# Kernel tuning notes

Hardware: AMD Instinct MI355X
Metric: run time of the kernel (lower is better)

The kernel has to match this reference:

```python
import jax, jax.numpy as jnp
import numpy as np

NUM_CHANNEL = 2                      # channels per telescope group
K = 7                                # hexagonal kernel size
N_LEV = [2048, 512, 128, 32, 8]      # pixels per level (stride-2 hex pooling ~ /4)
CHS = [2, 64, 128, 256, 512]         # channel progression n1->n_features->n2->n3->n4


def _iconv(x, idx, w, b):
    # x: [B,C,Nin], idx: [K,Nout], w: [O,C,K] -> [B,O,Nout]
    g = x[:, :, idx]                              # gather neighbours [B,C,K,Nout]
    return jnp.einsum('bckn,ock->bon', g, w) + b[None, :, None]


def _ipool(x, idx):
    # IndexedMaxPool2d: gather then max over kernel positions
    return x[:, :, idx].max(axis=2)               # [B,C,Nout]


def _bn(x, gamma, beta, eps=1e-5):
    # train-mode BatchNorm1d over (batch, pixel) dims, biased variance (torch semantics)
    m = x.mean(axis=(0, 2), keepdims=True)
    v = x.var(axis=(0, 2), keepdims=True)
    return (x - m) / jnp.sqrt(v + eps) * gamma[None, :, None] + beta[None, :, None]


def setup_inputs() -> dict:
    key = jax.random.key(0)
    ks = jax.random.split(key, 40)
    ki = iter(range(40))
    nk = lambda: ks[next(ki)]
    B = 256
    inp = {"x": jax.random.normal(nk(), (B, 2 * NUM_CHANNEL, N_LEV[0]), jnp.float32)}
    for i in range(4):
        inp[f"idx_conv{i+1}"] = jax.random.randint(nk(), (K, N_LEV[i]), 0, N_LEV[i])
        inp[f"idx_pool{i+1}"] = jax.random.randint(nk(), (K, N_LEV[i + 1]), 0, N_LEV[i])
        fan = float(CHS[i] * K)
        inp[f"w{i+1}"] = jax.random.normal(nk(), (CHS[i + 1], CHS[i], K), jnp.float32) / np.float32(np.sqrt(fan))
        inp[f"b{i+1}"] = jnp.zeros((CHS[i + 1],), jnp.float32)
        inp[f"gamma{i+1}"] = jnp.ones((CHS[i + 1],), jnp.float32)
        inp[f"beta{i+1}"] = jnp.zeros((CHS[i + 1],), jnp.float32)
    F = N_LEV[4] * CHS[4]            # 8 * 512 = 4096
    H = F // 2                       # 2048
    inp["lin1_w"] = jax.random.normal(nk(), (H, F), jnp.float32) / np.float32(np.sqrt(F))
    inp["lin1_b"] = jnp.zeros((H,), jnp.float32)
    inp["gamma5"] = jnp.ones((H,), jnp.float32)
    inp["beta5"] = jnp.zeros((H,), jnp.float32)
    inp["lin2_w"] = jax.random.normal(nk(), (3, H), jnp.float32) / np.float32(np.sqrt(H))
    inp["lin2_b"] = jnp.zeros((3,), jnp.float32)
    return inp


def reference(x, idx_conv1, idx_pool1, idx_conv2, idx_pool2, idx_conv3, idx_pool3,
              idx_conv4, idx_pool4, w1, b1, gamma1, beta1, w2, b2, gamma2, beta2,
              w3, b3, gamma3, beta3, w4, b4, gamma4, beta4,
              lin1_w, lin1_b, gamma5, beta5, lin2_w, lin2_b):
    layers = [(idx_conv1, idx_pool1, w1, b1, gamma1, beta1),
              (idx_conv2, idx_pool2, w2, b2, gamma2, beta2),
              (idx_conv3, idx_pool3, w3, b3, gamma3, beta3),
              (idx_conv4, idx_pool4, w4, b4, gamma4, beta4)]
    T = x.shape[1] // NUM_CHANNEL    # number of telescope groups (static)
    outs = []
    for i in range(T):
        o = x[:, i * NUM_CHANNEL:(i + 1) * NUM_CHANNEL, :]
        for (ic, ip, w, b, g, be) in layers:
            # conv -> pool -> bn -> relu (dropout with p=0 is identity)
            o = jax.nn.relu(_bn(_ipool(_iconv(o, ic, w, b), ip), g, be))
        outs.append(o)
    o = jnp.stack(outs, 1).mean(axis=1)          # [B, 512, 8]
    o = o.reshape(o.shape[0], -1)                # [B, 4096]
    o = o @ lin1_w.T + lin1_b                    # [B, 2048]
    m = o.mean(axis=0)
    v = o.var(axis=0)
    o = (o - m) / jnp.sqrt(v + 1e-5) * gamma5 + beta5
    o = jax.nn.relu(o)
    o = o @ lin2_w.T + lin2_b                    # [B, 3]
    cls = jax.nn.log_softmax(o[:, :2], axis=1)   # targets: class=2 (log-softmax), energy=1 (raw)
    return jnp.concatenate([cls, o[:, 2:3]], axis=1)
```

## Files before the change

### kernel.cpp

```cpp
#include <hip/hip_runtime.h>
#include <math.h>

#define B 256
#define KW 7

typedef __bf16 bf16x8 __attribute__((ext_vector_type(8)));
typedef __bf16 bf16x4 __attribute__((ext_vector_type(4)));
typedef float  f32x4  __attribute__((ext_vector_type(4)));

__device__ __forceinline__ void block_reduce2(float& s, float& s2, float* lds) {
    for (int off = 32; off > 0; off >>= 1) {
        s  += __shfl_down(s,  off, 64);
        s2 += __shfl_down(s2, off, 64);
    }
    int wave = threadIdx.x >> 6;
    int lane = threadIdx.x & 63;
    if (lane == 0) { lds[wave * 2] = s; lds[wave * 2 + 1] = s2; }
    __syncthreads();
    if (threadIdx.x == 0) {
        s  = lds[0] + lds[2] + lds[4] + lds[6];
        s2 = lds[1] + lds[3] + lds[5] + lds[7];
    }
}

__global__ __launch_bounds__(256) void k_transpose(const float* __restrict__ x,
                                                   float* __restrict__ A0) {
    int bid = blockIdx.x;
    int nt  = bid & 63;
    int rem = bid >> 6;
    int ci  = rem & 1;
    int t   = rem >> 1;
    int n0  = nt * 32;
    __shared__ float lds[32][257];
    int tid = threadIdx.x;
    int nl  = tid & 31;
    int bq  = tid >> 5;
    int ch  = t * 2 + ci;
    for (int p = 0; p < 32; p++) {
        int b = bq + p * 8;
        lds[nl][b] = x[((size_t)b * 4 + ch) * 2048 + n0 + nl];
    }
    __syncthreads();
    for (int nl2 = 0; nl2 < 32; nl2++) {
        A0[(((size_t)t * 2048 + n0 + nl2) * 2 + ci) * B + tid] = lds[nl2][tid];
    }
}

__global__ __launch_bounds__(256) void k_convpool1(
    const float* __restrict__ act,
    float* __restrict__ P1,
    const float* __restrict__ w,
    const float* __restrict__ bias,
    const int* __restrict__ idx_conv,
    const int* __restrict__ idx_pool,
    float* __restrict__ part1c)
{
    const int Kt = 14, C_out = 64, N_in = 2048, N_out = 512;
    int bid   = blockIdx.x;
    int cot   = bid & 1;
    int colid = bid >> 1;
    int t     = colid / N_out;
    int np    = colid - t * N_out;
    int co0   = cot << 5;

    __shared__ float lds_g[14 * 256];
    __shared__ float lds_w[14 * 33];
    __shared__ int   lds_idx[KW];

    int tid = threadIdx.x;
    int cog = tid >> 6;
    int bl  = tid & 63;

    float pmax[8][4];
    #pragma unroll
    for (int i = 0; i < 8; i++)
        #pragma unroll
        for (int j = 0; j < 4; j++) pmax[i][j] = -INFINITY;

    const float* actT = act + (size_t)t * N_in * 2 * B;

    for (int kp = 0; kp < KW; kp++) {
        int nc = idx_pool[kp * N_out + np];
        if (tid < KW) lds_idx[tid] = idx_conv[tid * N_in + nc];

        float acc[8][4];
        #pragma unroll
        for (int i = 0; i < 8; i++)
            #pragma unroll
            for (int j = 0; j < 4; j++) acc[i][j] = 0.f;

        __syncthreads();
        for (int e = tid; e < 32 * Kt; e += 256) {
            int kk = e % Kt;
            int co = e / Kt;
            lds_w[kk * 33 + co] = w[(size_t)(co0 + co) * Kt + kk];
        }
        for (int r = 0; r < Kt; r++) {
            int ci  = r / KW;
            int k   = r - ci * KW;
            int col = lds_idx[k];
            lds_g[r * 256 + tid] = actT[((size_t)col * 2 + ci) * B + tid];
        }
        __syncthreads();
        for (int kk = 0; kk < Kt; kk++) {
            float g0 = lds_g[kk * 256 + bl];
            float g1 = lds_g[kk * 256 + bl + 64];
            float g2 = lds_g[kk * 256 + bl + 128];
            float g3 = lds_g[kk * 256 + bl + 192];
            const float* wr = lds_w + kk * 33 + cog * 8;
            #pragma unroll
            for (int i = 0; i < 8; i++) {
                float wv = wr[i];
                acc[i][0] = fmaf(wv, g0, acc[i][0]);
                acc[i][1] = fmaf(wv, g1, acc[i][1]);
                acc[i][2] = fmaf(wv, g2, acc[i][2]);
                acc[i][3] = fmaf(wv, g3, acc[i][3]);
            }
        }
        #pragma unroll
        for (int i = 0; i < 8; i++)
            #pragma unroll
            for (int j = 0; j < 4; j++) pmax[i][j] = fmaxf(pmax[i][j], acc[i][j]);
    }

    float* outp = P1 + (((size_t)t * N_out + np) * C_out + co0) * B;
    float* pblk = part1c + (size_t)bid * 64;
    #pragma unroll
    for (int i = 0; i < 8; i++) {
        int co = cog * 8 + i;
        float bv = bias[co0 + co];
        float s = 0.f, s2 = 0.f;
        #pragma unroll
        for (int j = 0; j < 4; j++) {
            float val = pmax[i][j] + bv;
            outp[(size_t)co * B + bl + 64 * j] = val;
            s  += val;
            s2 += val * val;
        }
        for (int o = 32; o > 0; o >>= 1) {
            s  += __shfl_down(s,  o, 64);
            s2 += __shfl_down(s2, o, 64);
        }
        if ((tid & 63) == 0) {
            pblk[co]      = s;
            pblk[32 + co] = s2;
        }
    }
}

__global__ __launch_bounds__(256) void k_finstats1(
    const float* __restrict__ part1c,
    const float* __restrict__ gamma, const float* __restrict__ beta,
    float* __restrict__ scale, float* __restrict__ shift)
{
    int idx = blockIdx.x;
    int t = idx >> 6, c = idx & 63;
    int cot = c >> 5, cl = c & 31;
    float s = 0.f, s2 = 0.f;
    for (int np = threadIdx.x; np < 512; np += 256) {
        const float* pp = part1c + (size_t)((t * 512 + np) * 2 + cot) * 64;
        s  += pp[cl];
        s2 += pp[32 + cl];
    }
    __shared__ float lds[8];
    block_reduce2(s, s2, lds);
    if (threadIdx.x == 0) {
        float cnt  = 512.f * 256.f;
        float m    = s / cnt;
        float var  = s2 / cnt - m * m;
        float istd = rsqrtf(var + 1e-5f);
        float g    = gamma[c];
        scale[idx] = istd * g;
        shift[idx] = beta[c] - m * istd * g;
    }
}

__global__ __launch_bounds__(256) void k_bnrelu1t(
    const float* __restrict__ P1,
    const float* __restrict__ sc, const float* __restrict__ sh,
    __bf16* __restrict__ act1)
{
    int bid = blockIdx.x;
    int t = bid >> 9;
    int b = threadIdx.x;
    const float* src = P1 + (size_t)bid * 64 * B;
    __bf16* dst = act1 + (size_t)bid * B * 64 + (size_t)b * 64;
    const float* scp = sc + t * 64;
    const float* shp = sh + t * 64;
    __bf16 vals[64];
    #pragma unroll
    for (int co = 0; co < 64; co++) {
        float v = src[co * B + b];
        vals[co] = (__bf16)fmaxf(fmaf(v, scp[co], shp[co]), 0.f);
    }
    #pragma unroll
    for (int j = 0; j < 8; j++)
        *(bf16x8*)(dst + j * 8) = *(bf16x8*)&vals[j * 8];
}

__global__ void k_wr(const float* __restrict__ w, __bf16* __restrict__ wr,
                     int C_in, int total) {
    int idx = blockIdx.x * 256 + threadIdx.x;
    if (idx >= total) return;
    int ci = idx % C_in;
    int r  = idx / C_in;
    int kt = r % 7;
    int co = r / 7;
    wr[idx] = (__bf16)w[((size_t)co * C_in + ci) * 7 + kt];
}

__global__ void k_cvt8(const float* __restrict__ src, __bf16* __restrict__ dst, int total8) {
    int idx = blockIdx.x * 256 + threadIdx.x;
    if (idx >= total8) return;
    const f32x4* s4 = (const f32x4*)(src + (size_t)idx * 8);
    f32x4 a = s4[0], b = s4[1];
    bf16x8 v;
    v[0] = (__bf16)a[0]; v[1] = (__bf16)a[1]; v[2] = (__bf16)a[2]; v[3] = (__bf16)a[3];
    v[4] = (__bf16)b[0]; v[5] = (__bf16)b[1]; v[6] = (__bf16)b[2]; v[7] = (__bf16)b[3];
    *(bf16x8*)(dst + (size_t)idx * 8) = v;
}

__global__ __launch_bounds__(256) void k_conv_mfma(
    const __bf16* __restrict__ act,
    float* __restrict__ convo,
    const __bf16* __restrict__ wr,
    const int* __restrict__ idx_conv,
    int C_in, int C_out, int N, int ci_shift, int t0)
{
    int nco = C_out >> 6;
    int bid = blockIdx.x;
    int cot = bid % nco;
    int rem = bid / nco;
    int n    = rem % N;
    int tloc = rem / N;
    int t    = t0 + tloc;
    int co0  = cot * 64;
    int Kt   = C_in * KW;

    int tid  = threadIdx.x;
    int wv   = tid >> 6;
    int lane = tid & 63;
    int quad = lane >> 4;
    int lid  = lane & 15;

    f32x4 acc[4][4];
    #pragma unroll
    for (int i = 0; i < 4; i++)
        #pragma unroll
        for (int j = 0; j < 4; j++) {
            acc[i][j][0] = 0.f; acc[i][j][1] = 0.f;
            acc[i][j][2] = 0.f; acc[i][j][3] = 0.f;
        }

    const __bf16* actT = act + (size_t)t * N * B * C_in;
    const __bf16* wbase = wr + (size_t)(co0 + lid) * Kt + quad * 8;

    for (int k0 = 0; k0 < Kt; k0 += 32) {
        int kt  = k0 >> ci_shift;
        int ci0 = k0 & (C_in - 1);
        int col = idx_conv[kt * N + n];

        bf16x8 afrag[4];
        #pragma unroll
        for (int rt = 0; rt < 4; rt++)
            afrag[rt] = *(const bf16x8*)(wbase + (size_t)rt * 16 * Kt + k0);

        bf16x8 bfrag[4];
        const __bf16* gbase = actT + ((size_t)col * B + wv * 64 + lid) * C_in + ci0 + quad * 8;
        #pragma unroll
        for (int bt = 0; bt < 4; bt++)
            bfrag[bt] = *(const bf16x8*)(gbase + (size_t)bt * 16 * C_in);

        #pragma unroll
        for (int rt = 0; rt < 4; rt++)
            #pragma unroll
            for (int bt = 0; bt < 4; bt++)
                acc[rt][bt] = __builtin_amdgcn_mfma_f32_16x16x32_bf16(
                    afrag[rt], bfrag[bt], acc[rt][bt], 0, 0, 0);
    }

    float* outp = convo + ((size_t)(tloc * N + n) * B) * C_out;
    #pragma unroll
    for (int rt = 0; rt < 4; rt++)
        #pragma unroll
        for (int bt = 0; bt < 4; bt++) {
            int b  = wv * 64 + bt * 16 + lid;
            int co = co0 + rt * 16 + quad * 4;
            *(f32x4*)(outp + (size_t)b * C_out + co) = acc[rt][bt];
        }
}

__global__ __launch_bounds__(256) void k_poolstats(
    const float* __restrict__ convo,
    float* __restrict__ P,
    const float* __restrict__ bias,
    const int* __restrict__ idx_pool,
    float* __restrict__ part,
    int C, int N, int No, int t0)
{
    int bid  = blockIdx.x;
    int bg   = bid & 3;
    int rem  = bid >> 2;
    int np   = rem % No;
    int tloc = rem / No;
    int t    = t0 + tloc;
    int cols[7];
    #pragma unroll
    for (int k = 0; k < 7; k++) cols[k] = idx_pool[k * No + np];
    const float* base = convo + (size_t)tloc * N * B * C;
    float* pout = P + ((size_t)(t * No + np) * B) * C;
    int tid = threadIdx.x;
    float s[2] = {0.f, 0.f}, s2[2] = {0.f, 0.f};
    int NC, c0, bstart, bstep, nb;
    if (C >= 256) { NC = C >> 8; c0 = tid;           bstart = 0;        bstep = 1; nb = 64; }
    else          { NC = 1;      c0 = tid & (C - 1); bstart = tid >> 7; bstep = 2; nb = 32; }
    for (int j = 0; j < NC; j++) {
        int c = c0 + j * 256;
        float bv = bias[c];
        for (int i = 0; i < nb; i++) {
            int b = bg * 64 + bstart + i * bstep;
            float m = -1e30f;
            #pragma unroll
            for (int k = 0; k < 7; k++) {
                float v = base[((size_t)cols[k] * B + b) * C + c];
                m = fmaxf(m, v);
            }
            float val = m + bv;
            pout[(size_t)b * C + c] = val;
            s[j] += val; s2[j] += val * val;
        }
    }
    float* pp = part + (size_t)((t * No + np) * 4 + bg) * 1024;
    for (int j = 0; j < NC; j++) {
        pp[tid + j * 256]       = s[j];
        pp[512 + tid + j * 256] = s2[j];
    }
}

__global__ __launch_bounds__(256) void k_finstats(
    const float* __restrict__ part,
    const float* __restrict__ gamma, const float* __restrict__ beta,
    float* __restrict__ scale, float* __restrict__ shift,
    int C, int No)
{
    int idx = blockIdx.x;
    int t = idx / C, c = idx - t * C;
    int SMAX   = C < 256 ? 256 : C;
    int nslice = SMAX / C;
    int nblk   = No * 4;
    int total  = nblk * nslice;
    const float* pbase = part + (size_t)(t * No * 4) * 1024;
    float s = 0.f, s2 = 0.f;
    for (int e = threadIdx.x; e < total; e += 256) {
        int blk = e / nslice;
        int j   = e - blk * nslice;
        const float* pp = pbase + (size_t)blk * 1024;
        int sl = c + j * C;
        s  += pp[sl];
        s2 += pp[512 + sl];
    }
    __shared__ float lds[8];
    block_reduce2(s, s2, lds);
    if (threadIdx.x == 0) {
        float cnt  = (float)No * 256.f;
        float m    = s / cnt;
        float var  = s2 / cnt - m * m;
        float istd = rsqrtf(var + 1e-5f);
        float g    = gamma[c];
        scale[idx] = istd * g;
        shift[idx] = beta[c] - m * istd * g;
    }
}

__global__ void k_bnrelu(const float* __restrict__ P, __bf16* __restrict__ act,
                         const float* __restrict__ scale, const float* __restrict__ shift,
                         int C, int total)
{
    int idx = blockIdx.x * 256 + threadIdx.x;
    if (idx >= total) return;
    int c = idx & (C - 1);
    int t = idx >= (total >> 1) ? 1 : 0;
    int tc = t * C + c;
    float v = P[idx];
    act[idx] = (__bf16)fmaxf(fmaf(v, scale[tc], shift[tc]), 0.f);
}

__global__ __launch_bounds__(256) void k_zbuild(const float* __restrict__ P4,
                                                const float* __restrict__ sc4,
                                                const float* __restrict__ sh4,
                                                __bf16* __restrict__ z)
{
    int b = blockIdx.x;
    int tid = threadIdx.x;
    for (int j = 0; j < 2; j++) {
        int c = tid + j * 256;
        float s0 = sc4[c],       h0 = sh4[c];
        float s1 = sc4[512 + c], h1 = sh4[512 + c];
        #pragma unroll
        for (int np = 0; np < 8; np++) {
            float v0 = P4[(((size_t)0 * 8 + np) * B + b) * 512 + c];
            float v1 = P4[(((size_t)1 * 8 + np) * B + b) * 512 + c];
            float y0 = fmaxf(fmaf(v0, s0, h0), 0.f);
            float y1 = fmaxf(fmaf(v1, s1, h1), 0.f);
            z[(size_t)b * 4096 + c * 8 + np] = (__bf16)(0.5f * (y0 + y1));
        }
    }
}

__global__ __launch_bounds__(256) void k_lin1_part(
    const __bf16* __restrict__ zb,
    const __bf16* __restrict__ w1b,
    float* __restrict__ partL)
{
    int ht = blockIdx.x >> 3;
    int ks = blockIdx.x & 7;
    int h0 = ht * 64;
    int f_beg = ks * 512, f_end = f_beg + 512;

    int tid  = threadIdx.x;
    int wv   = tid >> 6;
    int lane = tid & 63;
    int quad = lane >> 4;
    int lid  = lane & 15;

    f32x4 acc[4][4];
    #pragma unroll
    for (int i = 0; i < 4; i++)
        #pragma unroll
        for (int j = 0; j < 4; j++) {
            acc[i][j][0] = 0.f; acc[i][j][1] = 0.f;
            acc[i][j][2] = 0.f; acc[i][j][3] = 0.f;
        }

    const __bf16* wbase = w1b + (size_t)(h0 + lid) * 4096 + quad * 8;
    const __bf16* zbase = zb + ((size_t)(wv * 64 + lid)) * 4096 + quad * 8;

    for (int f0 = f_beg; f0 < f_end; f0 += 32) {
        bf16x8 afrag[4];
        #pragma unroll
        for (int rt = 0; rt < 4; rt++)
            afrag[rt] = *(const bf16x8*)(wbase + (size_t)rt * 16 * 4096 + f0);
        bf16x8 bfrag[4];
        #pragma unroll
        for (int bt = 0; bt < 4; bt++)
            bfrag[bt] = *(const bf16x8*)(zbase + (size_t)bt * 16 * 4096 + f0);
        #pragma unroll
        for (int rt = 0; rt < 4; rt++)
            #pragma unroll
            for (int bt = 0; bt < 4; bt++)
                acc[rt][bt] = __builtin_amdgcn_mfma_f32_16x16x32_bf16(
                    afrag[rt], bfrag[bt], acc[rt][bt], 0, 0, 0);
    }
    float* outp = partL + (size_t)ks * 2048 * B;
    #pragma unroll
    for (int rt = 0; rt < 4; rt++)
        #pragma unroll
        for (int bt = 0; bt < 4; bt++) {
            int b = wv * 64 + bt * 16 + lid;
            int h = h0 + rt * 16 + quad * 4;
            #pragma unroll
            for (int r = 0; r < 4; r++)
                outp[(size_t)(h + r) * B + b] = acc[rt][bt][r];
        }
}

__global__ __launch_bounds__(256) void k_redstats5(
    const float* __restrict__ partL,
    const float* __restrict__ b1,
    const float* __restrict__ gamma5, const float* __restrict__ beta5,
    float* __restrict__ o1,
    float* __restrict__ scale5, float* __restrict__ shift5)
{
    int h = blockIdx.x;
    int b = threadIdx.x;
    float v = b1[h];
    #pragma unroll
    for (int s = 0; s < 8; s++)
        v += partL[((size_t)s * 2048 + h) * B + b];
    o1[(size_t)h * B + b] = v;
    float s1 = v, s2 = v * v;
    __shared__ float lds[8];
    block_reduce2(s1, s2, lds);
    if (threadIdx.x == 0) {
        float m    = s1 * (1.f / 256.f);
        float var  = s2 * (1.f / 256.f) - m * m;
        float istd = rsqrtf(var + 1e-5f);
        float g    = gamma5[h];
        scale5[h]  = istd * g;
        shift5[h]  = beta5[h] - m * istd * g;
    }
}

__global__ __launch_bounds__(256) void k_final(
    const float* __restrict__ o1,
    const float* __restrict__ scale5, const float* __restrict__ shift5,
    const float* __restrict__ w2, const float* __restrict__ b2,
    float* __restrict__ out)
{
    int b = blockIdx.x;
    int tid = threadIdx.x;
    float s0 = 0.f, s1 = 0.f, s2v = 0.f;
    for (int h = tid; h < 2048; h += 256) {
        float y = fmaxf(fmaf(o1[(size_t)h * B + b], scale5[h], shift5[h]), 0.f);
        s0  = fmaf(y, w2[h],        s0);
        s1  = fmaf(y, w2[2048 + h], s1);
        s2v = fmaf(y, w2[4096 + h], s2v);
    }
    for (int off = 32; off > 0; off >>= 1) {
        s0  += __shfl_down(s0,  off, 64);
        s1  += __shfl_down(s1,  off, 64);
        s2v += __shfl_down(s2v, off, 64);
    }
    __shared__ float lds[12];
    int wave = tid >> 6, lane = tid & 63;
    if (lane == 0) { lds[wave * 3] = s0; lds[wave * 3 + 1] = s1; lds[wave * 3 + 2] = s2v; }
    __syncthreads();
    if (tid == 0) {
        float o0 = lds[0] + lds[3] + lds[6] + lds[9]  + b2[0];
        float oa = lds[1] + lds[4] + lds[7] + lds[10] + b2[1];
        float ob = lds[2] + lds[5] + lds[8] + lds[11] + b2[2];
        float m   = fmaxf(o0, oa);
        float lse = m + logf(expf(o0 - m) + expf(oa - m));
        out[b * 3 + 0] = o0 - lse;
        out[b * 3 + 1] = oa - lse;
        out[b * 3 + 2] = ob;
    }
}

extern "C" void kernel_launch(void* const* d_in, const int* in_sizes, int n_in,
                              void* d_out, int out_size, void* d_ws, size_t ws_size,
                              hipStream_t stream) {
    (void)in_sizes; (void)n_in; (void)out_size; (void)ws_size;

    const float* x   = (const float*)d_in[0];
    const int*   ic1 = (const int*)d_in[1];
    const int*   ip1 = (const int*)d_in[2];
    const float* pW1 = (const float*)d_in[3];
    const float* pB1 = (const float*)d_in[4];
    const float* pG1 = (const float*)d_in[5];
    const float* pE1 = (const float*)d_in[6];
    const int*   ic2 = (const int*)d_in[7];
    const int*   ip2 = (const int*)d_in[8];
    const float* pW2 = (const float*)d_in[9];
    const float* pB2 = (const float*)d_in[10];
    const float* pG2 = (const float*)d_in[11];
    const float* pE2 = (const float*)d_in[12];
    const int*   ic3 = (const int*)d_in[13];
    const int*   ip3 = (const int*)d_in[14];
    const float* pW3 = (const float*)d_in[15];
    const float* pB3 = (const float*)d_in[16];
    const float* pG3 = (const float*)d_in[17];
    const float* pE3 = (const float*)d_in[18];
    const int*   ic4 = (const int*)d_in[19];
    const int*   ip4 = (const int*)d_in[20];
    const float* pW4 = (const float*)d_in[21];
    const float* pB4 = (const float*)d_in[22];
    const float* pG4 = (const float*)d_in[23];
    const float* pE4 = (const float*)d_in[24];
    const float* lw1 = (const float*)d_in[25];
    const float* lb1 = (const float*)d_in[26];
    const float* g5  = (const float*)d_in[27];
    const float* e5  = (const float*)d_in[28];
    const float* lw2 = (const float*)d_in[29];
    const float* lb2 = (const float*)d_in[30];

    char* ws = (char*)d_ws;
    size_t off = 0;
    auto alloc = [&](size_t bytes) -> char* {
        char* p = ws + off;
        off += (bytes + 511) & ~(size_t)511;
        return p;
    };

    float*  A0    = (float*) alloc((size_t)2 * 2048 * 2 * B * 4);
    __bf16* act1  = (__bf16*)alloc((size_t)2 * 512 * B * 64 * 2);
    char*   U     =          alloc((size_t)512 * B * 128 * 4);
    float*  P1f   = (float*)U;
    float*  convX = (float*)U;
    float*  partL = (float*)U;
    float*  Pf    = (float*) alloc((size_t)2 * 128 * B * 128 * 4);
    __bf16* actS  = (__bf16*)alloc((size_t)2 * 128 * B * 128 * 2);
    __bf16* Wr2   = (__bf16*)alloc((size_t)128 * 448 * 2);
    __bf16* Wr3   = (__bf16*)alloc((size_t)256 * 896 * 2);
    __bf16* Wr4   = (__bf16*)alloc((size_t)512 * 1792 * 2);
    __bf16* w1b   = (__bf16*)alloc((size_t)2048 * 4096 * 2);
    __bf16* z     = (__bf16*)alloc((size_t)256 * 4096 * 2);
    float*  o1    = (float*) alloc((size_t)2048 * B * 4);
    float*  part  = (float*) alloc((size_t)2 * 128 * 4 * 1024 * 4);
    float*  part1c= (float*) alloc((size_t)2048 * 64 * 4);
    float*  sc1 = (float*)alloc(2 * 64 * 4);
    float*  sh1 = (float*)alloc(2 * 64 * 4);
    float*  sc2 = (float*)alloc(2 * 128 * 4);
    float*  sh2 = (float*)alloc(2 * 128 * 4);
    float*  sc3 = (float*)alloc(2 * 256 * 4);
    float*  sh3 = (float*)alloc(2 * 256 * 4);
    float*  sc4 = (float*)alloc(2 * 512 * 4);
    float*  sh4 = (float*)alloc(2 * 512 * 4);
    float*  sc5 = (float*)alloc(2048 * 4);
    float*  sh5 = (float*)alloc(2048 * 4);

    k_wr<<<(128 * 448 + 255) / 256, 256, 0, stream>>>(pW2, Wr2, 64, 128 * 448);
    k_wr<<<(256 * 896 + 255) / 256, 256, 0, stream>>>(pW3, Wr3, 128, 256 * 896);
    k_wr<<<(512 * 1792 + 255) / 256, 256, 0, stream>>>(pW4, Wr4, 256, 512 * 1792);
    k_cvt8<<<(2048 * 4096 / 8) / 256, 256, 0, stream>>>(lw1, w1b, 2048 * 4096 / 8);

    k_transpose<<<256, 256, 0, stream>>>(x, A0);

    k_convpool1<<<2048, 256, 0, stream>>>(A0, P1f, pW1, pB1, ic1, ip1, part1c);
    k_finstats1<<<2 * 64, 256, 0, stream>>>(part1c, pG1, pE1, sc1, sh1);
    k_bnrelu1t<<<2 * 512, 256, 0, stream>>>(P1f, sc1, sh1, act1);

    for (int t = 0; t < 2; t++) {
        k_conv_mfma<<<2 * 512, 256, 0, stream>>>(act1, convX, Wr2, ic2, 64, 128, 512, 6, t);
        k_poolstats<<<128 * 4, 256, 0, stream>>>(convX, Pf, pB2, ip2, part, 128, 512, 128, t);
    }
    k_finstats<<<2 * 128, 256, 0, stream>>>(part, pG2, pE2, sc2, sh2, 128, 128);
    k_bnrelu<<<(2 * 128 * B * 128) / 256, 256, 0, stream>>>(Pf, actS, sc2, sh2, 128, 2 * 128 * B * 128);

    k_conv_mfma<<<4 * 128 * 2, 256, 0, stream>>>(actS, convX, Wr3, ic3, 128, 256, 128, 7, 0);
    k_poolstats<<<2 * 32 * 4, 256, 0, stream>>>(convX, Pf, pB3, ip3, part, 256, 128, 32, 0);
    k_finstats<<<2 * 256, 256, 0, stream>>>(part, pG3, pE3, sc3, sh3, 256, 32);
    k_bnrelu<<<(2 * 32 * B * 256) / 256, 256, 0, stream>>>(Pf, actS, sc3, sh3, 256, 2 * 32 * B * 256);

    k_conv_mfma<<<8 * 32 * 2, 256, 0, stream>>>(actS, convX, Wr4, ic4, 256, 512, 32, 8, 0);
    k_poolstats<<<2 * 8 * 4, 256, 0, stream>>>(convX, Pf, pB4, ip4, part, 512, 32, 8, 0);
    k_finstats<<<2 * 512, 256, 0, stream>>>(part, pG4, pE4, sc4, sh4, 512, 8);

    k_zbuild<<<256, 256, 0, stream>>>(Pf, sc4, sh4, z);
    k_lin1_part<<<256, 256, 0, stream>>>(z, w1b, partL);
    k_redstats5<<<2048, 256, 0, stream>>>(partL, lb1, g5, e5, o1, sc5, sh5);
    k_final<<<256, 256, 0, stream>>>(o1, sc5, sh5, lw2, lb2, (float*)d_out);
}
```

Before: 763.4 us.

## Store conv outputs in bf16, widen conv tile to 128 channels, merge group launches

The MFMA conv kernel now computes 128 output channels per block instead of 64. This halves the number of times each gathered activation fragment is reloaded, at the cost of more accumulator registers. The conv output buffer switches from fp32 to bf16, halving its write and pool-read traffic, and the pooling kernel converts values back to float when it reads them. Because the bf16 buffer is smaller, both telescope groups now fit in the shared workspace, so layer 2 runs as one conv and one pool launch instead of a per-group loop. The risk is lower occupancy from 128 accumulator VGPRs and a bf16 rounding error before max-pool and batch norm.

```diff
diff --git a/kernel.cpp b/kernel.cpp
--- a/kernel.cpp
+++ b/kernel.cpp
@@ -222,20 +222,19 @@
 
 __global__ __launch_bounds__(256) void k_conv_mfma(
     const __bf16* __restrict__ act,
-    float* __restrict__ convo,
+    __bf16* __restrict__ convo,
     const __bf16* __restrict__ wr,
     const int* __restrict__ idx_conv,
-    int C_in, int C_out, int N, int ci_shift, int t0)
-{
-    int nco = C_out >> 6;
+    int C_in, int C_out, int N, int ci_shift)
+{
+    int nco = C_out >> 7;
     int bid = blockIdx.x;
     int cot = bid % nco;
     int rem = bid / nco;
-    int n    = rem % N;
-    int tloc = rem / N;
-    int t    = t0 + tloc;
-    int co0  = cot * 64;
-    int Kt   = C_in * KW;
+    int n   = rem % N;
+    int t   = rem / N;
+    int co0 = cot * 128;
+    int Kt  = C_in * KW;
 
     int tid  = threadIdx.x;
     int wv   = tid >> 6;
@@ -243,9 +242,9 @@
     int quad = lane >> 4;
     int lid  = lane & 15;
 
-    f32x4 acc[4][4];
-    #pragma unroll
-    for (int i = 0; i < 4; i++)
+    f32x4 acc[8][4];
+    #pragma unroll
+    for (int i = 0; i < 8; i++)
         #pragma unroll
         for (int j = 0; j < 4; j++) {
             acc[i][j][0] = 0.f; acc[i][j][1] = 0.f;
@@ -260,11 +259,6 @@
         int ci0 = k0 & (C_in - 1);
         int col = idx_conv[kt * N + n];
 
-        bf16x8 afrag[4];
-        #pragma unroll
-        for (int rt = 0; rt < 4; rt++)
-            afrag[rt] = *(const bf16x8*)(wbase + (size_t)rt * 16 * Kt + k0);
-
         bf16x8 bfrag[4];
         const __bf16* gbase = actT + ((size_t)col * B + wv * 64 + lid) * C_in + ci0 + quad * 8;
         #pragma unroll
@@ -272,42 +266,48 @@
             bfrag[bt] = *(const bf16x8*)(gbase + (size_t)bt * 16 * C_in);
 
         #pragma unroll
-        for (int rt = 0; rt < 4; rt++)
+        for (int rt = 0; rt < 8; rt++) {
+            bf16x8 afrag = *(const bf16x8*)(wbase + (size_t)rt * 16 * Kt + k0);
             #pragma unroll
             for (int bt = 0; bt < 4; bt++)
                 acc[rt][bt] = __builtin_amdgcn_mfma_f32_16x16x32_bf16(
-                    afrag[rt], bfrag[bt], acc[rt][bt], 0, 0, 0);
-    }
-
-    float* outp = convo + ((size_t)(tloc * N + n) * B) * C_out;
-    #pragma unroll
-    for (int rt = 0; rt < 4; rt++)
+                    afrag, bfrag[bt], acc[rt][bt], 0, 0, 0);
+        }
+    }
+
+    __bf16* outp = convo + ((size_t)(t * N + n) * B) * C_out;
+    #pragma unroll
+    for (int rt = 0; rt < 8; rt++)
         #pragma unroll
         for (int bt = 0; bt < 4; bt++) {
             int b  = wv * 64 + bt * 16 + lid;
             int co = co0 + rt * 16 + quad * 4;
-            *(f32x4*)(outp + (size_t)b * C_out + co) = acc[rt][bt];
+            bf16x4 v;
+            v[0] = (__bf16)acc[rt][bt][0];
+            v[1] = (__bf16)acc[rt][bt][1];
+            v[2] = (__bf16)acc[rt][bt][2];
+            v[3] = (__bf16)acc[rt][bt][3];
+            *(bf16x4*)(outp + (size_t)b * C_out + co) = v;
         }
 }
 
 __global__ __launch_bounds__(256) void k_poolstats(
-    const float* __restrict__ convo,
+    const __bf16* __restrict__ convo,
     float* __restrict__ P,
     const float* __restrict__ bias,
     const int* __restrict__ idx_pool,
     float* __restrict__ part,
-    int C, int N, int No, int t0)
+    int C, int N, int No)
 {
     int bid  = blockIdx.x;
     int bg   = bid & 3;
     int rem  = bid >> 2;
     int np   = rem % No;
-    int tloc = rem / No;
-    int t    = t0 + tloc;
+    int t    = rem / No;
     int cols[7];
     #pragma unroll
     for (int k = 0; k < 7; k++) cols[k] = idx_pool[k * No + np];
-    const float* base = convo + (size_t)tloc * N * B * C;
+    const __bf16* base = convo + (size_t)t * N * B * C;
     float* pout = P + ((size_t)(t * No + np) * B) * C;
     int tid = threadIdx.x;
     float s[2] = {0.f, 0.f}, s2[2] = {0.f, 0.f};
@@ -322,7 +322,7 @@
             float m = -1e30f;
             #pragma unroll
             for (int k = 0; k < 7; k++) {
-                float v = base[((size_t)cols[k] * B + b) * C + c];
+                float v = (float)base[((size_t)cols[k] * B + b) * C + c];
                 m = fmaxf(m, v);
             }
             float val = m + bv;
@@ -576,7 +576,7 @@
     __bf16* act1  = (__bf16*)alloc((size_t)2 * 512 * B * 64 * 2);
     char*   U     =          alloc((size_t)512 * B * 128 * 4);
     float*  P1f   = (float*)U;
-    float*  convX = (float*)U;
+    __bf16* convX = (__bf16*)U;
     float*  partL = (float*)U;
     float*  Pf    = (float*) alloc((size_t)2 * 128 * B * 128 * 4);
     __bf16* actS  = (__bf16*)alloc((size_t)2 * 128 * B * 128 * 2);
@@ -610,20 +610,18 @@
     k_finstats1<<<2 * 64, 256, 0, stream>>>(part1c, pG1, pE1, sc1, sh1);
     k_bnrelu1t<<<2 * 512, 256, 0, stream>>>(P1f, sc1, sh1, act1);
 
-    for (int t = 0; t < 2; t++) {
-        k_conv_mfma<<<2 * 512, 256, 0, stream>>>(act1, convX, Wr2, ic2, 64, 128, 512, 6, t);
-        k_poolstats<<<128 * 4, 256, 0, stream>>>(convX, Pf, pB2, ip2, part, 128, 512, 128, t);
-    }
+    k_conv_mfma<<<1 * 512 * 2, 256, 0, stream>>>(act1, convX, Wr2, ic2, 64, 128, 512, 6);
+    k_poolstats<<<2 * 128 * 4, 256, 0, stream>>>(convX, Pf, pB2, ip2, part, 128, 512, 128);
     k_finstats<<<2 * 128, 256, 0, stream>>>(part, pG2, pE2, sc2, sh2, 128, 128);
     k_bnrelu<<<(2 * 128 * B * 128) / 256, 256, 0, stream>>>(Pf, actS, sc2, sh2, 128, 2 * 128 * B * 128);
 
-    k_conv_mfma<<<4 * 128 * 2, 256, 0, stream>>>(actS, convX, Wr3, ic3, 128, 256, 128, 7, 0);
-    k_poolstats<<<2 * 32 * 4, 256, 0, stream>>>(convX, Pf, pB3, ip3, part, 256, 128, 32, 0);
+    k_conv_mfma<<<2 * 128 * 2, 256, 0, stream>>>(actS, convX, Wr3, ic3, 128, 256, 128, 7);
+    k_poolstats<<<2 * 32 * 4, 256, 0, stream>>>(convX, Pf, pB3, ip3, part, 256, 128, 32);
     k_finstats<<<2 * 256, 256, 0, stream>>>(part, pG3, pE3, sc3, sh3, 256, 32);
     k_bnrelu<<<(2 * 32 * B * 256) / 256, 256, 0, stream>>>(Pf, actS, sc3, sh3, 256, 2 * 32 * B * 256);
 
-    k_conv_mfma<<<8 * 32 * 2, 256, 0, stream>>>(actS, convX, Wr4, ic4, 256, 512, 32, 8, 0);
-    k_poolstats<<<2 * 8 * 4, 256, 0, stream>>>(convX, Pf, pB4, ip4, part, 512, 32, 8, 0);
+    k_conv_mfma<<<4 * 32 * 2, 256, 0, stream>>>(actS, convX, Wr4, ic4, 256, 512, 32, 8);
+    k_poolstats<<<2 * 8 * 4, 256, 0, stream>>>(convX, Pf, pB4, ip4, part, 512, 32, 8);
     k_finstats<<<2 * 512, 256, 0, stream>>>(part, pG4, pE4, sc4, sh4, 512, 8);
 
     k_zbuild<<<256, 256, 0, stream>>>(Pf, sc4, sh4, z);
```

Result: faster. 702.9 us (-7.9%).
